# Kernel tuning notes

Hardware: AMD Instinct MI355X
Metric: run time of the kernel (lower is better)

The kernel has to match this reference:

```python
import jax, jax.numpy as jnp
import numpy as np

# --- static config (lmax = mmax = 2, m-prime coefficient layout) ---
L = 2
NCOEF = (L + 1) ** 2            # 9 coeffs; m-prime order: m=0 -> l=0,1,2 | m=1 -> (-,+) x l=1,2 | m=2 -> (-,+) x l=2
GATE_IDX = jnp.array([0, 1, 0, 1, 0, 1, 1, 1])  # (l-1) of each non-scalar coeff in m-prime order
N_NODES = 10000
N_EDGES = 50000
C_SPH = 128
C_HID = 128
C_EDGE = 128
EXTRA_M0 = L * C_HID            # gate scalars emitted by conv1's m=0 branch


def _silu(x):
    return x * jax.nn.sigmoid(x)


def _layernorm(x, g, b, eps=1e-5):
    mu = jnp.mean(x, axis=-1, keepdims=True)
    var = jnp.var(x, axis=-1, keepdims=True)
    return (x - mu) * jax.lax.rsqrt(var + eps) * g + b


def _radial(x_edge, w1, b1, g, beta, w2, b2):
    # RadialFunction: Linear -> LayerNorm -> SiLU -> Linear, emits per-edge channel weights [E, 6*c_in]
    h = _silu(_layernorm(x_edge @ w1 + b1, g, beta))
    return h @ w2 + b2


def _so2_conv(feat, rad, w0, b0, w1, w2, c_in, c_out, extra):
    # feat: [E, 9, c_in] in m-prime order. Block-diagonal SO2 conv with per-edge radial modulation.
    E = feat.shape[0]
    # m = 0 block (3 real coeffs) -> dense linear, optionally emits extra gating scalars
    x0 = feat[:, 0:3].reshape(E, 3 * c_in) * rad[:, : 3 * c_in]
    y0 = x0 @ w0 + b0                                   # [E, 3*c_out + extra]
    out0 = y0[:, : 3 * c_out].reshape(E, 3, c_out)
    x_extra = y0[:, 3 * c_out:]
    # m = 1 block: coeffs 3:7 -> [E, 2(sign), 2(l)*c_in], complex-structured matmul
    x1 = feat[:, 3:7].reshape(E, 2, 2 * c_in) * rad[:, 3 * c_in: 5 * c_in][:, None, :]
    y1 = x1 @ w1                                        # [E, 2, 4*c_out]
    h = 2 * c_out
    r, i = y1[..., :h], y1[..., h:]
    out1 = jnp.stack([r[:, 0] - i[:, 1], r[:, 1] + i[:, 0]], axis=1).reshape(E, 4, c_out)
    # m = 2 block: coeffs 7:9 -> [E, 2(sign), 1(l)*c_in]
    x2 = feat[:, 7:9].reshape(E, 2, c_in) * rad[:, 5 * c_in: 6 * c_in][:, None, :]
    y2 = x2 @ w2                                        # [E, 2, 2*c_out]
    r, i = y2[..., :c_out], y2[..., c_out:]
    out2 = jnp.stack([r[:, 0] - i[:, 1], r[:, 1] + i[:, 0]], axis=1).reshape(E, 2, c_out)
    return jnp.concatenate([out0, out1, out2], axis=1), x_extra


def _gate(gating, feat):
    # GateActivation (m_prime=True): SiLU on l=0 scalar, SiLU(gates) broadcast per-degree on l>0 coeffs
    E = feat.shape[0]
    g = _silu(gating).reshape(E, L, C_HID)[:, GATE_IDX]  # [E, 8, C_HID]
    return jnp.concatenate([_silu(feat[:, :1]), feat[:, 1:] * g], axis=1)


def setup_inputs() -> dict:
    key = jax.random.key(0)
    ks = jax.random.split(key, 16)

    def nrm(k, shape, scale=1.0):
        return jax.random.normal(k, shape, dtype=jnp.float32) * scale

    C, H, CE = C_SPH, C_HID, C_EDGE
    return {
        "x": nrm(ks[0], (N_NODES, NCOEF, C)),
        "x_edge": nrm(ks[1], (N_EDGES, CE)),
        "edge_distance": jax.random.uniform(ks[2], (N_EDGES,), dtype=jnp.float32),
        "edge_index": jax.random.randint(ks[3], (2, N_EDGES), 0, N_NODES),
        "wigner": nrm(ks[4], (N_EDGES, NCOEF, NCOEF), 0.3),
        "wigner_inv": nrm(ks[5], (N_EDGES, NCOEF, NCOEF), 0.3),
        # radial MLP 1 (edge embed -> 6*C_SPH per-edge weights)
        "rad1_w1": nrm(ks[6], (CE, CE), CE ** -0.5),
        "rad1_b1": jnp.zeros((CE,), jnp.float32),
        "rad1_g": jnp.ones((CE,), jnp.float32),
        "rad1_beta": jnp.zeros((CE,), jnp.float32),
        "rad1_w2": nrm(ks[7], (CE, 6 * C), CE ** -0.5),
        "rad1_b2": jnp.zeros((6 * C,), jnp.float32),
        # SO2 conv 1 (sphere -> hidden, + gate scalars)
        "c1_w0": nrm(ks[8], (3 * C, 3 * H + EXTRA_M0), (3 * C) ** -0.5),
        "c1_b0": jnp.zeros((3 * H + EXTRA_M0,), jnp.float32),
        "c1_w1": nrm(ks[9], (2 * C, 4 * H), (2 * C) ** -0.5),
        "c1_w2": nrm(ks[10], (C, 2 * H), C ** -0.5),
        # radial MLP 2 (edge embed -> 6*C_HID per-edge weights)
        "rad2_w1": nrm(ks[11], (CE, CE), CE ** -0.5),
        "rad2_b1": jnp.zeros((CE,), jnp.float32),
        "rad2_g": jnp.ones((CE,), jnp.float32),
        "rad2_beta": jnp.zeros((CE,), jnp.float32),
        "rad2_w2": nrm(ks[12], (CE, 6 * H), CE ** -0.5),
        "rad2_b2": jnp.zeros((6 * H,), jnp.float32),
        # SO2 conv 2 (hidden -> sphere)
        "c2_w0": nrm(ks[13], (3 * H, 3 * C), (3 * H) ** -0.5),
        "c2_b0": jnp.zeros((3 * C,), jnp.float32),
        "c2_w1": nrm(ks[14], (2 * H, 4 * C), (2 * H) ** -0.5),
        "c2_w2": nrm(ks[15], (H, 2 * C), H ** -0.5),
    }


def reference(x, x_edge, edge_distance, edge_index, wigner, wigner_inv,
              rad1_w1, rad1_b1, rad1_g, rad1_beta, rad1_w2, rad1_b2,
              c1_w0, c1_b0, c1_w1, c1_w2,
              rad2_w1, rad2_b1, rad2_g, rad2_beta, rad2_w2, rad2_b2,
              c2_w0, c2_b0, c2_w1, c2_w2):
    src, dst = edge_index[0], edge_index[1]
    # gather source node features + per-edge Wigner rotation into m-prime layout: [E, 9, C_SPH]
    msg = jnp.einsum('erf,efc->erc', wigner, x[src])
    rad1 = _radial(x_edge, rad1_w1, rad1_b1, rad1_g, rad1_beta, rad1_w2, rad1_b2)
    msg, gating = _so2_conv(msg, rad1, c1_w0, c1_b0, c1_w1, c1_w2, C_SPH, C_HID, EXTRA_M0)
    msg = _gate(gating, msg)
    rad2 = _radial(x_edge, rad2_w1, rad2_b1, rad2_g, rad2_beta, rad2_w2, rad2_b2)
    msg, _ = _so2_conv(msg, rad2, c2_w0, c2_b0, c2_w1, c2_w2, C_HID, C_SPH, 0)
    # rotate back to the global frame and scatter-sum onto destination nodes
    msg = jnp.einsum('efr,erc->efc', wigner_inv, msg)
    return jax.ops.segment_sum(msg, dst, num_segments=x.shape[0])
```

## Files before the change

### kernel.cpp

```cpp
#include <hip/hip_runtime.h>
#include <hip/hip_bf16.h>

#define EDGES 50000
#define NODES 10000

typedef __hip_bfloat16 bf16;
typedef __attribute__((ext_vector_type(8))) short bf16x8v;
typedef __attribute__((ext_vector_type(4))) float f32x4;

__device__ __forceinline__ float bf2f(bf16 v){ return __bfloat162float(v); }
__device__ __forceinline__ bf16  f2bf(float v){ return __float2bfloat16(v); }
__device__ __forceinline__ unsigned short f2bfu(float f){
  bf16 h = __float2bfloat16(f);
  union{ bf16 h; unsigned short s; } u; u.h = h; return u.s;
}
__device__ __forceinline__ float silu_f(float v){ return v * (1.0f/(1.0f+__expf(-v))); }

__device__ __forceinline__ unsigned mul1(unsigned a, unsigned b){
  union{unsigned u; float f;} a0,a1,b0,b1;
  a0.u = (a & 0xffffu) << 16; a1.u = a & 0xffff0000u;
  b0.u = (b & 0xffffu) << 16; b1.u = b & 0xffff0000u;
  float p0 = a0.f*b0.f, p1 = a1.f*b1.f;
  return (unsigned)f2bfu(p0) | ((unsigned)f2bfu(p1) << 16);
}
__device__ __forceinline__ uint4 mulp(uint4 a, uint4 b){
  uint4 r; r.x=mul1(a.x,b.x); r.y=mul1(a.y,b.y); r.z=mul1(a.z,b.z); r.w=mul1(a.w,b.w); return r;
}

__global__ __launch_bounds__(256)
void k_wT(const float* __restrict__ w, bf16* __restrict__ wt, int K, int N){
  __shared__ float tile[32][33];
  const int kb = blockIdx.x*32, nb = blockIdx.y*32;
  const int tx = threadIdx.x & 31, ty = threadIdx.x >> 5;
#pragma unroll
  for (int i=0;i<32;i+=8) tile[ty+i][tx] = w[(size_t)(kb+ty+i)*N + nb+tx];
  __syncthreads();
#pragma unroll
  for (int i=0;i<32;i+=8) wt[(size_t)(nb+ty+i)*K + kb+tx] = f2bf(tile[tx][ty+i]);
}

__global__ __launch_bounds__(128)
void k_gather_rot(const float* __restrict__ x, const int* __restrict__ eidx,
                  const float* __restrict__ wig, bf16* __restrict__ msg)
{
  const int e = blockIdx.x;
  const int c = threadIdx.x;
  __shared__ float wl[81];
  if (c < 81) wl[c] = wig[e*81 + c];
  const int src = eidx[e];
  const float* xp = x + (size_t)src*1152 + c;
  float xr[9];
#pragma unroll
  for (int f=0; f<9; ++f) xr[f] = xp[f*128];
  __syncthreads();
  bf16* mp = msg + (size_t)e*1152 + c;
#pragma unroll
  for (int fo=0; fo<9; ++fo){
    float a = 0.f;
#pragma unroll
    for (int f=0; f<9; ++f) a = fmaf(wl[fo*9+f], xr[f], a);
    mp[fo*128] = f2bf(a);
  }
}

__global__ __launch_bounds__(256)
void k_radial(const float* __restrict__ x_edge,
              const float* __restrict__ w1, const float* __restrict__ b1,
              const float* __restrict__ gm, const float* __restrict__ bt,
              const float* __restrict__ w2, const float* __restrict__ b2,
              bf16* __restrict__ ro)
{
  __shared__ float xe[16][128];
  __shared__ float h[16][128];
  __shared__ float mu_s[16], rs_s[16];
  const int t = threadIdx.x;
  const int e0 = blockIdx.x * 16;
  for (int i=0;i<8;++i){
    int lin = t + 256*i;
    int e = lin >> 7, j2 = lin & 127;
    xe[e][j2] = x_edge[(size_t)(e0+e)*128 + j2];
  }
  __syncthreads();
  const int j = t & 127, g = t >> 7;
  {
    float acc[8] = {0,0,0,0,0,0,0,0};
    for (int k=0;k<128;k+=4){
      float wv0 = w1[(k+0)*128+j];
      float wv1 = w1[(k+1)*128+j];
      float wv2 = w1[(k+2)*128+j];
      float wv3 = w1[(k+3)*128+j];
#pragma unroll
      for (int e=0;e<8;++e){
        float4 xv = *(const float4*)&xe[g*8+e][k];
        acc[e] += xv.x*wv0 + xv.y*wv1 + xv.z*wv2 + xv.w*wv3;
      }
    }
    float bv = b1[j];
#pragma unroll
    for (int e=0;e<8;++e) h[g*8+e][j] = acc[e] + bv;
  }
  __syncthreads();
  {
    int e = t >> 4, p = t & 15;
    float s=0.f, ss=0.f;
#pragma unroll
    for (int i=0;i<8;++i){ float v = h[e][p+16*i]; s += v; ss += v*v; }
#pragma unroll
    for (int off=8; off>0; off>>=1){ s += __shfl_xor(s, off, 16); ss += __shfl_xor(ss, off, 16); }
    if (p==0){
      float m = s*(1.f/128.f);
      mu_s[e] = m;
      rs_s[e] = rsqrtf(fmaxf(ss*(1.f/128.f)-m*m, 0.f) + 1e-5f);
    }
  }
  __syncthreads();
  {
    float gv = gm[j], bv = bt[j];
#pragma unroll
    for (int e=0;e<8;++e){
      int ee = g*8+e;
      float v = (h[ee][j]-mu_s[ee])*rs_s[ee]*gv + bv;
      h[ee][j] = silu_f(v);
    }
  }
  __syncthreads();
  if (t < 192){
    int col = t*4;
    float acc[16][4];
#pragma unroll
    for (int e=0;e<16;++e){ acc[e][0]=acc[e][1]=acc[e][2]=acc[e][3]=0.f; }
    for (int k=0;k<128;k+=4){
      float4 wv0 = *(const float4*)&w2[(k+0)*768+col];
      float4 wv1 = *(const float4*)&w2[(k+1)*768+col];
      float4 wv2 = *(const float4*)&w2[(k+2)*768+col];
      float4 wv3 = *(const float4*)&w2[(k+3)*768+col];
#pragma unroll
      for (int e=0;e<16;++e){
        float4 hv = *(const float4*)&h[e][k];
        acc[e][0] += hv.x*wv0.x + hv.y*wv1.x + hv.z*wv2.x + hv.w*wv3.x;
        acc[e][1] += hv.x*wv0.y + hv.y*wv1.y + hv.z*wv2.y + hv.w*wv3.y;
        acc[e][2] += hv.x*wv0.z + hv.y*wv1.z + hv.z*wv2.z + hv.w*wv3.z;
        acc[e][3] += hv.x*wv0.w + hv.y*wv1.w + hv.z*wv2.w + hv.w*wv3.w;
      }
    }
    float4 bv = *(const float4*)&b2[col];
#pragma unroll
    for (int e=0;e<16;++e){
      ushort4 pk;
      pk.x = f2bfu(acc[e][0]+bv.x);
      pk.y = f2bfu(acc[e][1]+bv.y);
      pk.z = f2bfu(acc[e][2]+bv.z);
      pk.w = f2bfu(acc[e][3]+bv.w);
      *reinterpret_cast<ushort4*>(&ro[(size_t)(e0+e)*768 + col]) = pk;
    }
  }
}

template<bool CONV1>
__global__ __launch_bounds__(256, 3)
void k_so2_mfma(const bf16* __restrict__ rad,
                const bf16* __restrict__ w0t, const float* __restrict__ b0,
                const bf16* __restrict__ w1t, const bf16* __restrict__ w2t,
                bf16* __restrict__ msg)
{
  __shared__ char ldsA[32768];
  __shared__ bf16 gls[8192];
  const int t    = threadIdx.x;
  const int lane = t & 63, wv = t >> 6;
  const int lrow = lane & 15, lhi = lane >> 4;
  const int e0 = blockIdx.x * 32;
  int evalid = EDGES - e0; if (evalid > 32) evalid = 32;
  const uint4 z4 = {0u,0u,0u,0u};

  uint4 mz0[6], rz0[6];
#pragma unroll
  for (int i=0;i<6;++i){
    int ch = t + 256*i;
    int row = ch / 48, k0 = (ch % 48) * 8;
    int e = e0 + row;
    mz0[i] = z4; rz0[i] = z4;
    if (e < EDGES){
      mz0[i] = *(const uint4*)(msg + (size_t)e*1152 + k0);
      rz0[i] = *(const uint4*)(rad + (size_t)e*768  + k0);
    }
  }
#pragma unroll
  for (int i=0;i<6;++i){
    int ch = t + 256*i;
    int row = ch / 48, k0 = (ch % 48) * 8;
    *(uint4*)(ldsA + ((row*768 + k0*2) ^ ((row&7)<<4))) = mulp(mz0[i], rz0[i]);
  }

  uint4 mz1[4], rz1[4];
#pragma unroll
  for (int i=0;i<4;++i){
    int ch = t + 256*i;
    int row = ch >> 5, k0 = (ch & 31) * 8;
    int e = e0 + (row >> 1);
    mz1[i] = z4; rz1[i] = z4;
    if (e < EDGES){
      mz1[i] = *(const uint4*)(msg + (size_t)e*1152 + 384 + (row&1)*256 + k0);
      rz1[i] = *(const uint4*)(rad + (size_t)e*768  + 384 + k0);
    }
  }
  __syncthreads();

  constexpr int NT0 = CONV1 ? 10 : 6;
  const int wcol0 = wv * NT0 * 16;
  f32x4 acc0[NT0][2];
  const f32x4 zf = {0.f,0.f,0.f,0.f};
#pragma unroll
  for (int nt=0; nt<NT0; ++nt){ acc0[nt][0]=zf; acc0[nt][1]=zf; }
  for (int ks=0; ks<12; ++ks){
    bf16x8v a0 = *(const bf16x8v*)(ldsA + (((lrow   )*768 + ks*64 + lhi*16) ^ ((lrow&7)<<4)));
    bf16x8v a1 = *(const bf16x8v*)(ldsA + (((16+lrow)*768 + ks*64 + lhi*16) ^ ((lrow&7)<<4)));
#pragma unroll
    for (int nt=0; nt<NT0; ++nt){
      int coln = wcol0 + nt*16 + lrow;
      bf16x8v b = *(const bf16x8v*)(w0t + (size_t)coln*384 + ks*32 + lhi*8);
      acc0[nt][0] = __builtin_amdgcn_mfma_f32_16x16x32_bf16(a0, b, acc0[nt][0], 0,0,0);
      acc0[nt][1] = __builtin_amdgcn_mfma_f32_16x16x32_bf16(a1, b, acc0[nt][1], 0,0,0);
    }
  }
  if (CONV1){
#pragma unroll
    for (int nt=0; nt<NT0; ++nt){
      int colb = wcol0 + nt*16;
      if (colb >= 384){
        float bc = b0[colb + lrow];
#pragma unroll
        for (int mt=0; mt<2; ++mt)
#pragma unroll
        for (int r=0; r<4; ++r){
          int el = mt*16 + lhi*4 + r;
          gls[el*256 + colb + lrow - 384] = f2bf(silu_f(acc0[nt][mt][r] + bc));
        }
      }
    }
  }
  __syncthreads();

  uint4 mz1b[4], rz1b[4];
#pragma unroll
  for (int i=0;i<4;++i){
    int ch = t + 256*i + 1024;
    int row = ch >> 5, k0 = (ch & 31) * 8;
    int e = e0 + (row >> 1);
    mz1b[i] = z4; rz1b[i] = z4;
    if (e < EDGES){
      mz1b[i] = *(const uint4*)(msg + (size_t)e*1152 + 384 + (row&1)*256 + k0);
      rz1b[i] = *(const uint4*)(rad + (size_t)e*768  + 384 + k0);
    }
  }

#pragma unroll
  for (int nt=0; nt<NT0; ++nt){
    int colb = wcol0 + nt*16;
    if (colb < 384){
      int col = colb + lrow;
      int f = col >> 7, c = col & 127;
      float bc = b0[col];
#pragma unroll
      for (int mt=0; mt<2; ++mt)
#pragma unroll
      for (int r=0; r<4; ++r){
        int el = mt*16 + lhi*4 + r;
        if (el < evalid){
          float v = acc0[nt][mt][r] + bc;
          float o;
          if (CONV1) o = (f==0) ? silu_f(v) : v * bf2f(gls[el*256 + (f==2?128:0) + c]);
          else       o = v;
          msg[(size_t)(e0+el)*1152 + col] = f2bf(o);
        }
      }
    }
  }

#pragma unroll
  for (int i=0;i<4;++i){
    int ch = t + 256*i;
    int row = ch >> 5, k0 = (ch & 31) * 8;
    *(uint4*)(ldsA + ((row*512 + k0*2) ^ ((row&7)<<4))) = mulp(mz1[i], rz1[i]);
  }
#pragma unroll
  for (int i=0;i<4;++i){
    int ch = t + 256*i + 1024;
    int row = ch >> 5, k0 = (ch & 31) * 8;
    *(uint4*)(ldsA + ((row*512 + k0*2) ^ ((row&7)<<4))) = mulp(mz1b[i], rz1b[i]);
  }

  uint4 mz2[4], rz2[4];
#pragma unroll
  for (int i=0;i<4;++i){
    int ch = t + 256*i;
    int row = ch >> 4, k0 = (ch & 15) * 8;
    int e = e0 + (row >> 1);
    mz2[i] = z4; rz2[i] = z4;
    if (e < EDGES){
      mz2[i] = *(const uint4*)(msg + (size_t)e*1152 + 896 + (row&1)*128 + k0);
      rz2[i] = *(const uint4*)(rad + (size_t)e*768  + 640 + k0);
    }
  }
  __syncthreads();

#pragma unroll
  for (int half=0; half<2; ++half){
    f32x4 acc1[4][2][2];
#pragma unroll
    for (int p=0;p<4;++p){ acc1[p][0][0]=zf; acc1[p][0][1]=zf; acc1[p][1][0]=zf; acc1[p][1][1]=zf; }
    for (int ks=0; ks<8; ++ks){
      bf16x8v aA[2];
#pragma unroll
      for (int m2=0; m2<2; ++m2){
        int row = (half*2+m2)*16 + lrow;
        aA[m2] = *(const bf16x8v*)(ldsA + ((row*512 + ks*64 + lhi*16) ^ ((row&7)<<4)));
      }
#pragma unroll
      for (int p=0; p<4; ++p){
        int jj = wv*64 + p*16 + lrow;
        bf16x8v br = *(const bf16x8v*)(w1t + (size_t)jj*256       + ks*32 + lhi*8);
        bf16x8v bi = *(const bf16x8v*)(w1t + (size_t)(jj+256)*256 + ks*32 + lhi*8);
#pragma unroll
        for (int m2=0;m2<2;++m2){
          acc1[p][m2][0] = __builtin_amdgcn_mfma_f32_16x16x32_bf16(aA[m2], br, acc1[p][m2][0], 0,0,0);
          acc1[p][m2][1] = __builtin_amdgcn_mfma_f32_16x16x32_bf16(aA[m2], bi, acc1[p][m2][1], 0,0,0);
        }
      }
    }
#pragma unroll
    for (int p=0;p<4;++p)
#pragma unroll
    for (int m2=0;m2<2;++m2){
      int mt = half*2 + m2;
#pragma unroll
      for (int re=0;re<2;++re){
        int el = mt*8 + lhi*2 + re;
        float r0 = acc1[p][m2][0][2*re+0], r1 = acc1[p][m2][0][2*re+1];
        float i0 = acc1[p][m2][1][2*re+0], i1 = acc1[p][m2][1][2*re+1];
        float o0 = r0 - i1, o1 = r1 + i0;
        int jj = wv*64 + p*16 + lrow;
        if (CONV1){ float g = bf2f(gls[el*256 + jj]); o0 *= g; o1 *= g; }
        if (el < evalid){
          size_t base = (size_t)(e0+el)*1152;
          msg[base + 384 + jj] = f2bf(o0);
          msg[base + 640 + jj] = f2bf(o1);
        }
      }
    }
  }
  __syncthreads();

#pragma unroll
  for (int i=0;i<4;++i){
    int ch = t + 256*i;
    int row = ch >> 4, k0 = (ch & 15) * 8;
    *(uint4*)(ldsA + ((row*256 + k0*2) ^ ((row&7)<<4))) = mulp(mz2[i], rz2[i]);
  }
  __syncthreads();

  {
    f32x4 acc2[2][4][2];
#pragma unroll
    for (int p=0;p<2;++p)
#pragma unroll
    for (int mt=0;mt<4;++mt){ acc2[p][mt][0]=zf; acc2[p][mt][1]=zf; }
    for (int ks=0; ks<4; ++ks){
      bf16x8v aA[4];
#pragma unroll
      for (int mt=0;mt<4;++mt){
        int row = mt*16 + lrow;
        aA[mt] = *(const bf16x8v*)(ldsA + ((row*256 + ks*64 + lhi*16) ^ ((row&7)<<4)));
      }
#pragma unroll
      for (int p=0;p<2;++p){
        int jj = wv*32 + p*16 + lrow;
        bf16x8v br = *(const bf16x8v*)(w2t + (size_t)jj*128       + ks*32 + lhi*8);
        bf16x8v bi = *(const bf16x8v*)(w2t + (size_t)(jj+128)*128 + ks*32 + lhi*8);
#pragma unroll
        for (int mt=0;mt<4;++mt){
          acc2[p][mt][0] = __builtin_amdgcn_mfma_f32_16x16x32_bf16(aA[mt], br, acc2[p][mt][0], 0,0,0);
          acc2[p][mt][1] = __builtin_amdgcn_mfma_f32_16x16x32_bf16(aA[mt], bi, acc2[p][mt][1], 0,0,0);
        }
      }
    }
#pragma unroll
    for (int p=0;p<2;++p)
#pragma unroll
    for (int mt=0;mt<4;++mt)
#pragma unroll
    for (int re=0;re<2;++re){
      int el = mt*8 + lhi*2 + re;
      float r0 = acc2[p][mt][0][2*re+0], r1 = acc2[p][mt][0][2*re+1];
      float i0 = acc2[p][mt][1][2*re+0], i1 = acc2[p][mt][1][2*re+1];
      float o0 = r0 - i1, o1 = r1 + i0;
      int jj = wv*32 + p*16 + lrow;
      if (CONV1){ float g = bf2f(gls[el*256 + 128 + jj]); o0 *= g; o1 *= g; }
      if (el < evalid){
        size_t base = (size_t)(e0+el)*1152;
        msg[base + 896  + jj] = f2bf(o0);
        msg[base + 1024 + jj] = f2bf(o1);
      }
    }
  }
}

__global__ __launch_bounds__(128)
void k_wiginv_scatter(const bf16* __restrict__ msg, const int* __restrict__ eidx,
                      const float* __restrict__ wiginv, float* __restrict__ out)
{
  const int e = blockIdx.x;
  const int c = threadIdx.x;
  __shared__ float wl[81];
  if (c < 81) wl[c] = wiginv[e*81 + c];
  float m[9];
#pragma unroll
  for (int r=0;r<9;++r) m[r] = bf2f(msg[(size_t)e*1152 + r*128 + c]);
  const int dst = eidx[EDGES + e];
  __syncthreads();
  float* op = out + (size_t)dst*1152 + c;
#pragma unroll
  for (int f=0;f<9;++f){
    float a = 0.f;
#pragma unroll
    for (int r=0;r<9;++r) a = fmaf(wl[f*9+r], m[r], a);
    atomicAdd(op + f*128, a);
  }
}

extern "C" void kernel_launch(void* const* d_in, const int* in_sizes, int n_in,
                              void* d_out, int out_size, void* d_ws, size_t ws_size,
                              hipStream_t stream)
{
  const float* x       = (const float*)d_in[0];
  const float* x_edge  = (const float*)d_in[1];
  const int*   eidx    = (const int*)  d_in[3];
  const float* wig     = (const float*)d_in[4];
  const float* wiginv  = (const float*)d_in[5];
  const float* r1w1    = (const float*)d_in[6];
  const float* r1b1    = (const float*)d_in[7];
  const float* r1g     = (const float*)d_in[8];
  const float* r1bt    = (const float*)d_in[9];
  const float* r1w2    = (const float*)d_in[10];
  const float* r1b2    = (const float*)d_in[11];
  const float* c1w0    = (const float*)d_in[12];
  const float* c1b0    = (const float*)d_in[13];
  const float* c1w1    = (const float*)d_in[14];
  const float* c1w2    = (const float*)d_in[15];
  const float* r2w1    = (const float*)d_in[16];
  const float* r2b1    = (const float*)d_in[17];
  const float* r2g     = (const float*)d_in[18];
  const float* r2bt    = (const float*)d_in[19];
  const float* r2w2    = (const float*)d_in[20];
  const float* r2b2    = (const float*)d_in[21];
  const float* c2w0    = (const float*)d_in[22];
  const float* c2b0    = (const float*)d_in[23];
  const float* c2w1    = (const float*)d_in[24];
  const float* c2w2    = (const float*)d_in[25];
  float* out = (float*)d_out;

  char* ws = (char*)d_ws;
  bf16* msg  = (bf16*)(ws);
  bf16* rad  = (bf16*)(ws + (size_t)115200000);
  bf16* w0t1 = (bf16*)(ws + (size_t)192000000);
  bf16* w1t1 = (bf16*)(ws + (size_t)192491520);
  bf16* w2t1 = (bf16*)(ws + (size_t)192753664);
  bf16* w0t2 = (bf16*)(ws + (size_t)192819200);
  bf16* w1t2 = (bf16*)(ws + (size_t)193114112);
  bf16* w2t2 = (bf16*)(ws + (size_t)193376256);

  k_wT<<<dim3(12,20),256,0,stream>>>(c1w0, w0t1, 384, 640);
  k_wT<<<dim3( 8,16),256,0,stream>>>(c1w1, w1t1, 256, 512);
  k_wT<<<dim3( 4, 8),256,0,stream>>>(c1w2, w2t1, 128, 256);
  k_wT<<<dim3(12,12),256,0,stream>>>(c2w0, w0t2, 384, 384);
  k_wT<<<dim3( 8,16),256,0,stream>>>(c2w1, w1t2, 256, 512);
  k_wT<<<dim3( 4, 8),256,0,stream>>>(c2w2, w2t2, 128, 256);

  hipMemsetAsync(d_out, 0, (size_t)out_size*sizeof(float), stream);
  k_gather_rot<<<EDGES, 128, 0, stream>>>(x, eidx, wig, msg);
  k_radial<<<EDGES/16, 256, 0, stream>>>(x_edge, r1w1, r1b1, r1g, r1bt, r1w2, r1b2, rad);
  k_so2_mfma<true ><<<(EDGES+31)/32, 256, 0, stream>>>(rad, w0t1, c1b0, w1t1, w2t1, msg);
  k_radial<<<EDGES/16, 256, 0, stream>>>(x_edge, r2w1, r2b1, r2g, r2bt, r2w2, r2b2, rad);
  k_so2_mfma<false><<<(EDGES+31)/32, 256, 0, stream>>>(rad, w0t2, c2b0, w1t2, w2t2, msg);
  k_wiginv_scatter<<<EDGES, 128, 0, stream>>>(msg, eidx, wiginv, out);
}
```

Measured before the change: 1.474 ms.

## Stage SO2 conv outputs through LDS for coalesced 16-byte stores; batch B loads

The m=0, m=1 and m=2 output epilogues now write their results into LDS first and then copy them to global memory as 16-byte vector stores per edge row. Before, each lane wrote scattered 2-byte bf16 values straight to global memory. The weight (B) fragments for each k-step are also loaded into register arrays before the MFMA loops, so the load latency can overlap with the matrix math. In exchange, the kernel gains extra __syncthreads barriers and LDS reuse, and may use more registers.

```diff
diff --git a/kernel.cpp b/kernel.cpp
--- a/kernel.cpp
+++ b/kernel.cpp
@@ -171,6 +171,7 @@
   const int e0 = blockIdx.x * 32;
   int evalid = EDGES - e0; if (evalid > 32) evalid = 32;
   const uint4 z4 = {0u,0u,0u,0u};
+  const f32x4 zf = {0.f,0.f,0.f,0.f};
 
   uint4 mz0[6], rz0[6];
 #pragma unroll
@@ -206,20 +207,28 @@
   __syncthreads();
 
   constexpr int NT0 = CONV1 ? 10 : 6;
+  constexpr int HB  = NT0 / 2;
   const int wcol0 = wv * NT0 * 16;
   f32x4 acc0[NT0][2];
-  const f32x4 zf = {0.f,0.f,0.f,0.f};
 #pragma unroll
   for (int nt=0; nt<NT0; ++nt){ acc0[nt][0]=zf; acc0[nt][1]=zf; }
   for (int ks=0; ks<12; ++ks){
     bf16x8v a0 = *(const bf16x8v*)(ldsA + (((lrow   )*768 + ks*64 + lhi*16) ^ ((lrow&7)<<4)));
     bf16x8v a1 = *(const bf16x8v*)(ldsA + (((16+lrow)*768 + ks*64 + lhi*16) ^ ((lrow&7)<<4)));
 #pragma unroll
-    for (int nt=0; nt<NT0; ++nt){
-      int coln = wcol0 + nt*16 + lrow;
-      bf16x8v b = *(const bf16x8v*)(w0t + (size_t)coln*384 + ks*32 + lhi*8);
-      acc0[nt][0] = __builtin_amdgcn_mfma_f32_16x16x32_bf16(a0, b, acc0[nt][0], 0,0,0);
-      acc0[nt][1] = __builtin_amdgcn_mfma_f32_16x16x32_bf16(a1, b, acc0[nt][1], 0,0,0);
+    for (int h=0; h<2; ++h){
+      bf16x8v bb[HB];
+#pragma unroll
+      for (int j=0;j<HB;++j){
+        int coln = wcol0 + (h*HB+j)*16 + lrow;
+        bb[j] = *(const bf16x8v*)(w0t + (size_t)coln*384 + ks*32 + lhi*8);
+      }
+#pragma unroll
+      for (int j=0;j<HB;++j){
+        int nt = h*HB+j;
+        acc0[nt][0] = __builtin_amdgcn_mfma_f32_16x16x32_bf16(a0, bb[j], acc0[nt][0], 0,0,0);
+        acc0[nt][1] = __builtin_amdgcn_mfma_f32_16x16x32_bf16(a1, bb[j], acc0[nt][1], 0,0,0);
+      }
     }
   }
   if (CONV1){
@@ -253,28 +262,41 @@
     }
   }
 
-#pragma unroll
-  for (int nt=0; nt<NT0; ++nt){
-    int colb = wcol0 + nt*16;
-    if (colb < 384){
-      int col = colb + lrow;
-      int f = col >> 7, c = col & 127;
-      float bc = b0[col];
-#pragma unroll
-      for (int mt=0; mt<2; ++mt)
-#pragma unroll
-      for (int r=0; r<4; ++r){
-        int el = mt*16 + lhi*4 + r;
-        if (el < evalid){
+  {
+    bf16* y0 = (bf16*)ldsA;
+#pragma unroll
+    for (int nt=0; nt<NT0; ++nt){
+      int colb = wcol0 + nt*16;
+      if (colb < 384){
+        int col = colb + lrow;
+        int f = col >> 7, c = col & 127;
+        float bc = b0[col];
+#pragma unroll
+        for (int mt=0; mt<2; ++mt)
+#pragma unroll
+        for (int r=0; r<4; ++r){
+          int el = mt*16 + lhi*4 + r;
           float v = acc0[nt][mt][r] + bc;
           float o;
           if (CONV1) o = (f==0) ? silu_f(v) : v * bf2f(gls[el*256 + (f==2?128:0) + c]);
           else       o = v;
-          msg[(size_t)(e0+el)*1152 + col] = f2bf(o);
+          y0[el*392 + col] = f2bf(o);
         }
       }
     }
   }
+  __syncthreads();
+  {
+    const bf16* y0 = (const bf16*)ldsA;
+#pragma unroll
+    for (int i=0;i<6;++i){
+      int idx = t + 256*i;
+      int el = idx / 48, rem = idx - el*48;
+      if (el < evalid)
+        *(uint4*)(msg + (size_t)(e0+el)*1152 + rem*8) = *(const uint4*)&y0[el*392 + rem*8];
+    }
+  }
+  __syncthreads();
 
 #pragma unroll
   for (int i=0;i<4;++i){
@@ -315,40 +337,55 @@
         int row = (half*2+m2)*16 + lrow;
         aA[m2] = *(const bf16x8v*)(ldsA + ((row*512 + ks*64 + lhi*16) ^ ((row&7)<<4)));
       }
+      bf16x8v br[4], bi[4];
 #pragma unroll
       for (int p=0; p<4; ++p){
         int jj = wv*64 + p*16 + lrow;
-        bf16x8v br = *(const bf16x8v*)(w1t + (size_t)jj*256       + ks*32 + lhi*8);
-        bf16x8v bi = *(const bf16x8v*)(w1t + (size_t)(jj+256)*256 + ks*32 + lhi*8);
-#pragma unroll
-        for (int m2=0;m2<2;++m2){
-          acc1[p][m2][0] = __builtin_amdgcn_mfma_f32_16x16x32_bf16(aA[m2], br, acc1[p][m2][0], 0,0,0);
-          acc1[p][m2][1] = __builtin_amdgcn_mfma_f32_16x16x32_bf16(aA[m2], bi, acc1[p][m2][1], 0,0,0);
-        }
-      }
-    }
-#pragma unroll
-    for (int p=0;p<4;++p)
-#pragma unroll
-    for (int m2=0;m2<2;++m2){
-      int mt = half*2 + m2;
+        br[p] = *(const bf16x8v*)(w1t + (size_t)jj*256       + ks*32 + lhi*8);
+        bi[p] = *(const bf16x8v*)(w1t + (size_t)(jj+256)*256 + ks*32 + lhi*8);
+      }
+#pragma unroll
+      for (int p=0; p<4; ++p)
+#pragma unroll
+      for (int m2=0;m2<2;++m2){
+        acc1[p][m2][0] = __builtin_amdgcn_mfma_f32_16x16x32_bf16(aA[m2], br[p], acc1[p][m2][0], 0,0,0);
+        acc1[p][m2][1] = __builtin_amdgcn_mfma_f32_16x16x32_bf16(aA[m2], bi[p], acc1[p][m2][1], 0,0,0);
+      }
+    }
+    __syncthreads();
+    {
+      bf16* y1 = (bf16*)ldsA;
+#pragma unroll
+      for (int p=0;p<4;++p)
+#pragma unroll
+      for (int m2=0;m2<2;++m2)
 #pragma unroll
       for (int re=0;re<2;++re){
-        int el = mt*8 + lhi*2 + re;
+        int elL = m2*8 + lhi*2 + re;
+        int el  = half*16 + elL;
         float r0 = acc1[p][m2][0][2*re+0], r1 = acc1[p][m2][0][2*re+1];
         float i0 = acc1[p][m2][1][2*re+0], i1 = acc1[p][m2][1][2*re+1];
         float o0 = r0 - i1, o1 = r1 + i0;
         int jj = wv*64 + p*16 + lrow;
         if (CONV1){ float g = bf2f(gls[el*256 + jj]); o0 *= g; o1 *= g; }
-        if (el < evalid){
-          size_t base = (size_t)(e0+el)*1152;
-          msg[base + 384 + jj] = f2bf(o0);
-          msg[base + 640 + jj] = f2bf(o1);
-        }
-      }
-    }
-  }
-  __syncthreads();
+        y1[elL*512 + jj]       = f2bf(o0);
+        y1[elL*512 + 256 + jj] = f2bf(o1);
+      }
+    }
+    __syncthreads();
+    {
+      const bf16* y1 = (const bf16*)ldsA;
+#pragma unroll
+      for (int i=0;i<4;++i){
+        int idx = t + 256*i;
+        int elL = idx >> 6, c0 = (idx & 63) * 8;
+        int el = half*16 + elL;
+        if (el < evalid)
+          *(uint4*)(msg + (size_t)(e0+el)*1152 + 384 + c0) = *(const uint4*)&y1[elL*512 + c0];
+      }
+    }
+    __syncthreads();
+  }
 
 #pragma unroll
   for (int i=0;i<4;++i){
@@ -371,34 +408,49 @@
         int row = mt*16 + lrow;
         aA[mt] = *(const bf16x8v*)(ldsA + ((row*256 + ks*64 + lhi*16) ^ ((row&7)<<4)));
       }
+      bf16x8v br2[2], bi2[2];
 #pragma unroll
       for (int p=0;p<2;++p){
         int jj = wv*32 + p*16 + lrow;
-        bf16x8v br = *(const bf16x8v*)(w2t + (size_t)jj*128       + ks*32 + lhi*8);
-        bf16x8v bi = *(const bf16x8v*)(w2t + (size_t)(jj+128)*128 + ks*32 + lhi*8);
-#pragma unroll
-        for (int mt=0;mt<4;++mt){
-          acc2[p][mt][0] = __builtin_amdgcn_mfma_f32_16x16x32_bf16(aA[mt], br, acc2[p][mt][0], 0,0,0);
-          acc2[p][mt][1] = __builtin_amdgcn_mfma_f32_16x16x32_bf16(aA[mt], bi, acc2[p][mt][1], 0,0,0);
-        }
-      }
-    }
-#pragma unroll
-    for (int p=0;p<2;++p)
-#pragma unroll
-    for (int mt=0;mt<4;++mt)
-#pragma unroll
-    for (int re=0;re<2;++re){
-      int el = mt*8 + lhi*2 + re;
-      float r0 = acc2[p][mt][0][2*re+0], r1 = acc2[p][mt][0][2*re+1];
-      float i0 = acc2[p][mt][1][2*re+0], i1 = acc2[p][mt][1][2*re+1];
-      float o0 = r0 - i1, o1 = r1 + i0;
-      int jj = wv*32 + p*16 + lrow;
-      if (CONV1){ float g = bf2f(gls[el*256 + 128 + jj]); o0 *= g; o1 *= g; }
-      if (el < evalid){
-        size_t base = (size_t)(e0+el)*1152;
-        msg[base + 896  + jj] = f2bf(o0);
-        msg[base + 1024 + jj] = f2bf(o1);
+        br2[p] = *(const bf16x8v*)(w2t + (size_t)jj*128       + ks*32 + lhi*8);
+        bi2[p] = *(const bf16x8v*)(w2t + (size_t)(jj+128)*128 + ks*32 + lhi*8);
+      }
+#pragma unroll
+      for (int p=0;p<2;++p)
+#pragma unroll
+      for (int mt=0;mt<4;++mt){
+        acc2[p][mt][0] = __builtin_amdgcn_mfma_f32_16x16x32_bf16(aA[mt], br2[p], acc2[p][mt][0], 0,0,0);
+        acc2[p][mt][1] = __builtin_amdgcn_mfma_f32_16x16x32_bf16(aA[mt], bi2[p], acc2[p][mt][1], 0,0,0);
+      }
+    }
+    __syncthreads();
+    {
+      bf16* y2 = (bf16*)ldsA;
+#pragma unroll
+      for (int p=0;p<2;++p)
+#pragma unroll
+      for (int mt=0;mt<4;++mt)
+#pragma unroll
+      for (int re=0;re<2;++re){
+        int el = mt*8 + lhi*2 + re;
+        float r0 = acc2[p][mt][0][2*re+0], r1 = acc2[p][mt][0][2*re+1];
+        float i0 = acc2[p][mt][1][2*re+0], i1 = acc2[p][mt][1][2*re+1];
+        float o0 = r0 - i1, o1 = r1 + i0;
+        int jj = wv*32 + p*16 + lrow;
+        if (CONV1){ float g = bf2f(gls[el*256 + 128 + jj]); o0 *= g; o1 *= g; }
+        y2[el*264 + jj]       = f2bf(o0);
+        y2[el*264 + 128 + jj] = f2bf(o1);
+      }
+    }
+    __syncthreads();
+    {
+      const bf16* y2 = (const bf16*)ldsA;
+#pragma unroll
+      for (int i=0;i<4;++i){
+        int idx = t + 256*i;
+        int el = idx >> 5, c0 = (idx & 31) * 8;
+        if (el < evalid)
+          *(uint4*)(msg + (size_t)(e0+el)*1152 + 896 + c0) = *(const uint4*)&y2[el*264 + c0];
       }
     }
   }
```

After: 1.461 ms. Within noise of the previous version (-0.9%).
